# Kernel optimization log

Hardware: AMD Instinct MI355X
Metric: run time of the kernel (lower is better)

The kernel has to match this reference:

```python
import jax, jax.numpy as jnp
import numpy as np


def setup_inputs() -> dict:
    key = jax.random.key(0)
    B, T_TEXT, MAX_LEN = 32, 512, 4096
    # per-token durations in frames, uniform in [1, 8) -> repeats in {1..8}
    durations = jax.random.uniform(key, (B, T_TEXT), dtype=jnp.float32, minval=1.0, maxval=8.0)
    return {"durations": durations, "max_len": MAX_LEN}


def reference(durations, max_len):
    # Faithful translation of Variance_Block.Length_Regulate:
    #   repeats = (durations.float() + 0.5).long()          (truncation == round for positive d)
    #   reps_cumsum = cumsum(pad(repeats, left=1))
    #   align[b, t, j] = (cumsum[:, j] <= t) & (cumsum[:, j+1] > t)
    repeats = (durations + 0.5).astype(jnp.int32)            # [B, T_text]
    ends = jnp.cumsum(repeats, axis=1)                       # reps_cumsum[:, 1:]
    starts = ends - repeats                                  # reps_cumsum[:, :-1]
    range_ = jnp.arange(max_len, dtype=jnp.int32)            # [max_len]
    # [B, max_len, T_text] boolean alignment via broadcast compare
    alignments = (starts[:, None, :] <= range_[None, :, None]) & (ends[:, None, :] > range_[None, :, None])
    return alignments.astype(jnp.float32)
```

## Files before the change

### kernel.cpp

```cpp
#include <hip/hip_runtime.h>


#define T_TEXT 512

__global__ __launch_bounds__(T_TEXT) void lr_scan_scatter(
        const float* __restrict__ dur,
        float* __restrict__ out,
        int max_len) {
    __shared__ int s[T_TEXT];
    const int b = blockIdx.x;
    const int tid = threadIdx.x;

    const int rep = (int)(dur[b * T_TEXT + tid] + 0.5f);
    s[tid] = rep;
    __syncthreads();

    for (int off = 1; off < T_TEXT; off <<= 1) {
        int v = s[tid];
        int add = (tid >= off) ? s[tid - off] : 0;
        __syncthreads();
        s[tid] = v + add;
        __syncthreads();
    }

    int end = s[tid];
    int start = end - rep;
    if (end > max_len) end = max_len;

    float* col = out + ((size_t)b * max_len) * T_TEXT + tid;
    for (int t = start; t < end; ++t) {
        col[(size_t)t * T_TEXT] = 1.0f;
    }
}

extern "C" void kernel_launch(void* const* d_in, const int* in_sizes, int n_in,
                              void* d_out, int out_size, void* d_ws, size_t ws_size,
                              hipStream_t stream) {
    const float* dur = (const float*)d_in[0];
    float* out = (float*)d_out;

    const int BT = in_sizes[0];
    const int B = BT / T_TEXT;
    const int max_len = out_size / BT;

    hipMemsetAsync(d_out, 0, (size_t)out_size * sizeof(float), stream);

    lr_scan_scatter<<<B, T_TEXT, 0, stream>>>(dur, out, max_len);
}
```

Before: 253.9 us.

## Replace memset-plus-scatter with inverse index map and single dense fill pass

Computes per-frame token index into a workspace via the scan kernel, then writes the whole alignment tensor in one coalesced float4 pass that places the single 1.0 per row inline. This removes the separate full-output memset and the strided per-column scatter writes. It adds a small workspace write/read and a second kernel launch, and depends on sufficient workspace being provided.

```diff
diff --git a/kernel.cpp b/kernel.cpp
--- a/kernel.cpp
+++ b/kernel.cpp
@@ -2,6 +2,61 @@
 
 
 #define T_TEXT 512
+#define RB 32
+#define WTHR 256
+
+__global__ __launch_bounds__(T_TEXT) void lr_scan_inv(
+        const float* __restrict__ dur,
+        int* __restrict__ inv,
+        int max_len) {
+    __shared__ int s[T_TEXT];
+    const int b = blockIdx.x;
+    const int tid = threadIdx.x;
+
+    const int rep = (int)(dur[b * T_TEXT + tid] + 0.5f);
+    s[tid] = rep;
+    __syncthreads();
+    for (int off = 1; off < T_TEXT; off <<= 1) {
+        int v = s[tid];
+        int add = (tid >= off) ? s[tid - off] : 0;
+        __syncthreads();
+        s[tid] = v + add;
+        __syncthreads();
+    }
+    int end = s[tid];
+    int start = end - rep;
+    int total = s[T_TEXT - 1];
+    if (end > max_len) end = max_len;
+
+    int* invb = inv + b * max_len;
+    for (int t = start; t < end; ++t) invb[t] = tid;
+    for (int t = total + tid; t < max_len; t += T_TEXT) invb[t] = -1;
+}
+
+__global__ __launch_bounds__(WTHR) void lr_fill(
+        const int* __restrict__ inv,
+        float* __restrict__ out,
+        int max_len) {
+    const int b = blockIdx.y;
+    const int t0 = blockIdx.x * RB;
+    const int tid = threadIdx.x;
+
+    const int* invb = inv + b * max_len + t0;
+    float4* outv = (float4*)(out + ((size_t)b * max_len + t0) * T_TEXT);
+    const int rows = (max_len - t0 < RB) ? (max_len - t0) : RB;
+    const int nvec = rows * (T_TEXT / 4);
+
+    #pragma unroll 4
+    for (int f = tid; f < nvec; f += WTHR) {
+        int r = f >> 7;
+        int c = (f & 127) << 2;
+        int j = invb[r];
+        float4 v = make_float4(0.f, 0.f, 0.f, 0.f);
+        int d = j - c;
+        if ((unsigned)d < 4u) ((float*)&v)[d] = 1.0f;
+        outv[f] = v;
+    }
+}
 
 __global__ __launch_bounds__(T_TEXT) void lr_scan_scatter(
         const float* __restrict__ dur,
@@ -10,11 +65,9 @@
     __shared__ int s[T_TEXT];
     const int b = blockIdx.x;
     const int tid = threadIdx.x;
-
     const int rep = (int)(dur[b * T_TEXT + tid] + 0.5f);
     s[tid] = rep;
     __syncthreads();
-
     for (int off = 1; off < T_TEXT; off <<= 1) {
         int v = s[tid];
         int add = (tid >= off) ? s[tid - off] : 0;
@@ -22,15 +75,11 @@
         s[tid] = v + add;
         __syncthreads();
     }
-
     int end = s[tid];
     int start = end - rep;
     if (end > max_len) end = max_len;
-
     float* col = out + ((size_t)b * max_len) * T_TEXT + tid;
-    for (int t = start; t < end; ++t) {
-        col[(size_t)t * T_TEXT] = 1.0f;
-    }
+    for (int t = start; t < end; ++t) col[(size_t)t * T_TEXT] = 1.0f;
 }
 
 extern "C" void kernel_launch(void* const* d_in, const int* in_sizes, int n_in,
@@ -43,7 +92,15 @@
     const int B = BT / T_TEXT;
     const int max_len = out_size / BT;
 
-    hipMemsetAsync(d_out, 0, (size_t)out_size * sizeof(float), stream);
+    const size_t inv_bytes = (size_t)B * max_len * sizeof(int);
 
-    lr_scan_scatter<<<B, T_TEXT, 0, stream>>>(dur, out, max_len);
+    if (ws_size >= inv_bytes) {
+        int* inv = (int*)d_ws;
+        lr_scan_inv<<<B, T_TEXT, 0, stream>>>(dur, inv, max_len);
+        dim3 grid((max_len + RB - 1) / RB, B);
+        lr_fill<<<grid, WTHR, 0, stream>>>(inv, out, max_len);
+    } else {
+        hipMemsetAsync(d_out, 0, (size_t)out_size * sizeof(float), stream);
+        lr_scan_scatter<<<B, T_TEXT, 0, stream>>>(dur, out, max_len);
+    }
 }
```

Result: slower. 264.8 us (+4.3%).
